# Kernel optimization log

Hardware: AMD Instinct MI355X
Metric: run time of the kernel (lower is better)

## Reference

```python
import jax, jax.numpy as jnp
import numpy as np

N_FFT = 4096
HOP = 1024
EPS = 1e-10


def hann(n):
    # periodic Hann window, matches torch.hann_window(n)
    return 0.5 - 0.5 * jnp.cos(2.0 * jnp.pi * jnp.arange(n) / n)


def stft(x, window):
    # x: (..., T) real -> (..., F, frames) complex; center=True, reflect pad, onesided
    pad = N_FFT // 2
    x = jnp.pad(x, [(0, 0)] * (x.ndim - 1) + [(pad, pad)], mode='reflect')
    n_frames = 1 + (x.shape[-1] - N_FFT) // HOP
    idx = jnp.arange(n_frames)[:, None] * HOP + jnp.arange(N_FFT)[None, :]
    frames = x[..., idx] * window  # (..., frames, N_FFT)
    return jnp.swapaxes(jnp.fft.rfft(frames, axis=-1), -1, -2)  # (..., F, frames)


def istft(spec, window, length):
    # spec: (..., F, frames) complex -> (..., length) real; torch.istft semantics (center=True)
    frames = jnp.fft.irfft(jnp.swapaxes(spec, -1, -2), n=N_FFT, axis=-1) * window
    n_frames = frames.shape[-2]
    out_len = N_FFT + HOP * (n_frames - 1)
    idx = (jnp.arange(n_frames)[:, None] * HOP + jnp.arange(N_FFT)[None, :]).reshape(-1)
    flat = frames.reshape(frames.shape[:-2] + (-1,))
    y = jnp.zeros(frames.shape[:-2] + (out_len,), frames.dtype).at[..., idx].add(flat)
    wsq = jnp.zeros((out_len,), frames.dtype).at[idx].add(jnp.tile(window ** 2, n_frames))
    y = y / jnp.where(wsq > 1e-11, wsq, 1.0)
    pad = N_FFT // 2
    return y[..., pad:pad + length]


def setup_inputs() -> dict:
    key = jax.random.key(0)
    k1, k2, k3 = jax.random.split(key, 3)
    audio = jax.random.normal(k1, (2, 2, 441000), jnp.float32)
    W = jax.random.normal(k2, (4, 2049, 2049), jnp.float32) * 0.02
    b = jax.random.normal(k3, (4, 2049), jnp.float32) * 0.01
    return {"audio": audio, "W": W, "b": b}


def reference(audio, W, b):
    window = hann(N_FFT).astype(audio.dtype)
    mix = stft(audio, window)                 # (N, C, F, T) complex64
    X = jnp.abs(mix)                          # ComplexNorm, mono=False, power=1
    Xd = jax.lax.stop_gradient(X)             # Separator feeds X.detach() to target models
    # target models: per-target linear over frequency bins + ReLU (nonneg spectrogram)
    V = jax.nn.relu(jnp.einsum('ncft,jgf->njcgt', Xd, W) + b[None, :, None, :, None])
    # wiener(iterations=0, softmask=False, residual=False): y_j = v_j * exp(i*angle(mix))
    phase = mix / (jnp.abs(mix) + EPS)        # unit-magnitude complex
    Y = V.astype(phase.real.dtype) * phase[:, None]  # (N, J, C, F, T) complex
    estimates = istft(Y, window, audio.shape[-1])    # (N, J, C, T_audio)
    return estimates
```

## Files before the change

kernel.cpp:

```cpp
#include <hip/hip_runtime.h>
#include <hip/hip_bf16.h>
#include <math.h>

#define T_AUDIO 441000
#define NH   2048
#define HOP  1024
#define NBINS 2049
#define NFRAMES 431
#define PAD  2048

#define GP  2176
#define KP  2112
#define TPN 512

#define NBLK 108
#define SPAN 7168

#define TWO_PI 6.2831853071795864769f

#define PADI(i) ((i) + ((i) >> 4))

typedef __bf16 bf16_t;
typedef bf16_t bf16x8 __attribute__((ext_vector_type(8)));
typedef bf16_t bf16x4 __attribute__((ext_vector_type(4)));
typedef float f32x4 __attribute__((ext_vector_type(4)));
typedef _Float16 h16;
typedef h16 h16x4 __attribute__((ext_vector_type(4)));

__device__ __forceinline__ unsigned pack_bf2(float a, float b) {
    union { bf16_t h; unsigned short u; } ca, cb;
    ca.h = (bf16_t)a; cb.h = (bf16_t)b;
    return (unsigned)ca.u | ((unsigned)cb.u << 16);
}
__device__ __forceinline__ float2 unpack_bf2(unsigned v) {
    union { unsigned u; float f; } a, b;
    a.u = v << 16;
    b.u = v & 0xffff0000u;
    return make_float2(a.f, b.f);
}

__device__ __forceinline__ float2 cadd(float2 a, float2 b) { return make_float2(a.x + b.x, a.y + b.y); }
__device__ __forceinline__ float2 csub(float2 a, float2 b) { return make_float2(a.x - b.x, a.y - b.y); }
__device__ __forceinline__ float2 cmul(float2 a, float2 b) {
    return make_float2(a.x * b.x - a.y * b.y, a.x * b.y + a.y * b.x);
}
__device__ __forceinline__ float2 cmulc(float2 u, float2 w) {
    return make_float2(u.x * w.x + u.y * w.y, u.y * w.x - u.x * w.y);
}

__global__ void k_tab(float2* __restrict__ tw) {
    int i = blockIdx.x * 256 + threadIdx.x;
    if (i < 4096) {
        float s, c;
        sincosf((float)i * (TWO_PI / 4096.0f), &s, &c);
        tw[i] = make_float2(c, s);
    }
}

template<bool FWD>
__device__ __forceinline__ void fft2048_reg8(float2* x, int tid,
                                             const float2* __restrict__ tw) {
    const float sgn = FWD ? -1.0f : 1.0f;
    const float R2 = 0.70710678118654752440f;
    int s = 1, ls = 0, fac = 2;
    #pragma unroll
    for (int st = 0; st < 3; st++) {
        int q = tid & (s - 1);
        int p = tid >> ls;
        int e = p * fac;
        float2 w[7];
        #pragma unroll
        for (int k = 0; k < 7; k++) w[k] = tw[e * (k + 1)];
        float2 v[8];
        #pragma unroll
        for (int k = 0; k < 8; k++) v[k] = x[PADI(tid + 256 * k)];
        __syncthreads();
        float2 s0 = cadd(v[0], v[4]), s1 = cadd(v[1], v[5]),
               s2 = cadd(v[2], v[6]), s3 = cadd(v[3], v[7]);
        float2 d0 = csub(v[0], v[4]), d1 = csub(v[1], v[5]),
               d2 = csub(v[2], v[6]), d3 = csub(v[3], v[7]);
        float2 X0, X1, X2, X3, X4, X5, X6, X7;
        {
            float2 t0 = cadd(s0, s2), t1 = csub(s0, s2);
            float2 t2 = cadd(s1, s3), t3 = csub(s1, s3);
            float2 it3 = make_float2(-sgn * t3.y, sgn * t3.x);
            X0 = cadd(t0, t2); X4 = csub(t0, t2);
            X2 = cadd(t1, it3); X6 = csub(t1, it3);
        }
        {
            float2 e0 = d0;
            float2 e1 = make_float2(R2 * (d1.x - sgn * d1.y), R2 * (sgn * d1.x + d1.y));
            float2 e2 = make_float2(-sgn * d2.y, sgn * d2.x);
            float2 e3 = make_float2(-R2 * (d3.x + sgn * d3.y), R2 * (sgn * d3.x - d3.y));
            float2 t0 = cadd(e0, e2), t1 = csub(e0, e2);
            float2 t2 = cadd(e1, e3), t3 = csub(e1, e3);
            float2 it3 = make_float2(-sgn * t3.y, sgn * t3.x);
            X1 = cadd(t0, t2); X5 = csub(t0, t2);
            X3 = cadd(t1, it3); X7 = csub(t1, it3);
        }
        int ob = q + 8 * s * p;
        x[PADI(ob)] = X0;
        float2 XX[7] = {X1, X2, X3, X4, X5, X6, X7};
        #pragma unroll
        for (int k = 0; k < 7; k++) {
            float2 u = XX[k];
            x[PADI(ob + s * (k + 1))] = FWD ? cmulc(u, w[k]) : cmul(w[k], u);
        }
        __syncthreads();
        s <<= 3; ls += 3; fac <<= 3;
    }
    {
        float2 v[8];
        #pragma unroll
        for (int k = 0; k < 8; k++) v[k] = x[PADI(tid + 256 * k)];
        __syncthreads();
        #pragma unroll
        for (int h = 0; h < 2; h++) {
            float2 c0 = v[h], c1 = v[h + 2], c2 = v[h + 4], c3 = v[h + 6];
            float2 t0 = cadd(c0, c2), t1 = csub(c0, c2);
            float2 t2 = cadd(c1, c3), t3 = csub(c1, c3);
            float2 it3 = make_float2(-sgn * t3.y, sgn * t3.x);
            int base = tid + 256 * h;
            x[PADI(base)]        = cadd(t0, t2);
            x[PADI(base + 512)]  = cadd(t1, it3);
            x[PADI(base + 1024)] = csub(t0, t2);
            x[PADI(base + 1536)] = csub(t1, it3);
        }
        __syncthreads();
    }
}

__global__ __launch_bounds__(256) void k_stft(const float* __restrict__ audio,
        bf16_t* __restrict__ Xb, unsigned* __restrict__ ph,
        const float2* __restrict__ tw) {
    __shared__ float2 buf[2176];
    int blk = blockIdx.x;
    int nc = blk / NFRAMES;
    int fr = blk - nc * NFRAMES;
    const float* a = audio + (size_t)nc * T_AUDIO;
    int tid = threadIdx.x;
    int base = fr * HOP - PAD;
    #pragma unroll
    for (int it = 0; it < 8; it++) {
        int m = tid + it * 256;
        int r0 = base + 2 * m;
        int r1 = r0 + 1;
        r0 = r0 < 0 ? -r0 : (r0 >= T_AUDIO ? 2 * T_AUDIO - 2 - r0 : r0);
        r1 = r1 < 0 ? -r1 : (r1 >= T_AUDIO ? 2 * T_AUDIO - 2 - r1 : r1);
        float4 tt = ((const float4*)tw)[m];
        float x0 = a[r0] * (0.5f - 0.5f * tt.x);
        float x1 = a[r1] * (0.5f - 0.5f * tt.z);
        buf[PADI(m)] = make_float2(x0, x1);
    }
    __syncthreads();
    fft2048_reg8<true>(buf, tid, tw);
    size_t orow = ((size_t)nc * NFRAMES + fr) * KP;
    bf16_t* Xrow = Xb + ((size_t)nc * TPN + fr) * KP;
    for (int k = tid; k < NBINS; k += 256) {
        float2 Zk = buf[PADI(k & 2047)];
        float2 Zm = buf[PADI((2048 - k) & 2047)];
        float ex = 0.5f * (Zk.x + Zm.x), ey = 0.5f * (Zk.y - Zm.y);
        float ox = 0.5f * (Zk.y + Zm.y), oy = -0.5f * (Zk.x - Zm.x);
        float2 w = tw[k];
        float re = ex + w.x * ox + w.y * oy;
        float im = ey + w.x * oy - w.y * ox;
        float mag = sqrtf(re * re + im * im);
        float inv = 1.0f / (mag + 1e-10f);
        Xrow[k] = (bf16_t)mag;
        ph[orow + k] = pack_bf2(re * inv, im * inv);
    }
}

__global__ __launch_bounds__(256) void k_convW(const float* __restrict__ W,
        bf16_t* __restrict__ Wb) {
    size_t idx = (size_t)blockIdx.x * 256 + threadIdx.x;
    size_t total = (size_t)4 * GP * KP / 8;
    if (idx >= total) return;
    size_t e = idx * 8;
    int f0 = (int)(e % KP);
    size_t rem = e / KP;
    int g = (int)(rem % GP);
    int j = (int)(rem / GP);
    bf16x8 v = {};
    if (g < NBINS) {
        const float* src = W + ((size_t)j * NBINS + g) * NBINS;
        #pragma unroll
        for (int r = 0; r < 8; r++) {
            int f = f0 + r;
            v[r] = (bf16_t)(f < NBINS ? src[f] : 0.0f);
        }
    }
    *(bf16x8*)(Wb + e) = v;
}

__global__ __launch_bounds__(256) void k_gemm_mfma(const bf16_t* __restrict__ Wb,
        const float* __restrict__ bias, const bf16_t* __restrict__ Xb,
        bf16_t* __restrict__ V) {
    __shared__ bf16_t As[128 * 64];
    __shared__ bf16_t Bs[64 * 64];
    int id = blockIdx.x;
    int xcd = id & 7, nn = id >> 3;
    int G = xcd + 8 * (nn / 28);
    if (G >= 68) return;
    int m28 = nn % 28;
    int j  = G / 17;
    int g0 = (G % 17) * 128;
    int nc = m28 / 7;
    int t0 = (m28 % 7) * 64;
    const bf16_t* A = Wb + ((size_t)j * GP + g0) * KP;
    const bf16_t* B = Xb + ((size_t)nc * TPN + t0) * KP;
    int tid = threadIdx.x;
    int lane = tid & 63, wid = tid >> 6;
    int wm = wid >> 1, wn = wid & 1;

    const bf16_t* srcA[4];
    #pragma unroll
    for (int i = 0; i < 4; i++) {
        int s = i * 256 + tid;
        int r = s >> 3, cc = (s & 7) ^ (r & 7);
        srcA[i] = A + (size_t)r * KP + cc * 8;
    }
    const bf16_t* srcB[2];
    #pragma unroll
    for (int i = 0; i < 2; i++) {
        int s = i * 256 + tid;
        int r = s >> 3, cc = (s & 7) ^ (r & 7);
        srcB[i] = B + (size_t)r * KP + cc * 8;
    }

    int laneLo = lane & 15, laneHi = lane >> 4;
    int offA[4][2], offB[2][2];
    #pragma unroll
    for (int mm = 0; mm < 4; mm++) {
        int r = wm * 64 + mm * 16 + laneLo;
        #pragma unroll
        for (int kk = 0; kk < 2; kk++) {
            int c = kk * 4 + laneHi;
            offA[mm][kk] = r * 128 + ((c ^ (r & 7)) << 4);
        }
    }
    #pragma unroll
    for (int n = 0; n < 2; n++) {
        int r = wn * 32 + n * 16 + laneLo;
        #pragma unroll
        for (int kk = 0; kk < 2; kk++) {
            int c = kk * 4 + laneHi;
            offB[n][kk] = r * 128 + ((c ^ (r & 7)) << 4);
        }
    }

    f32x4 acc[4][2];
    #pragma unroll
    for (int mm = 0; mm < 4; mm++)
        #pragma unroll
        for (int n = 0; n < 2; n++)
            acc[mm][n] = (f32x4){0.f, 0.f, 0.f, 0.f};

    for (int k0 = 0; k0 < KP; k0 += 64) {
        #pragma unroll
        for (int i = 0; i < 4; i++)
            __builtin_amdgcn_global_load_lds(
                (const __attribute__((address_space(1))) void*)(srcA[i] + k0),
                (__attribute__((address_space(3))) void*)(As + (i * 256 + tid) * 8),
                16, 0, 0);
        #pragma unroll
        for (int i = 0; i < 2; i++)
            __builtin_amdgcn_global_load_lds(
                (const __attribute__((address_space(1))) void*)(srcB[i] + k0),
                (__attribute__((address_space(3))) void*)(Bs + (i * 256 + tid) * 8),
                16, 0, 0);
        __syncthreads();

        bf16x8 af[4][2], bfr[2][2];
        #pragma unroll
        for (int mm = 0; mm < 4; mm++)
            #pragma unroll
            for (int kk = 0; kk < 2; kk++)
                af[mm][kk] = *(const bf16x8*)((const char*)As + offA[mm][kk]);
        #pragma unroll
        for (int n = 0; n < 2; n++)
            #pragma unroll
            for (int kk = 0; kk < 2; kk++)
                bfr[n][kk] = *(const bf16x8*)((const char*)Bs + offB[n][kk]);
        #pragma unroll
        for (int mm = 0; mm < 4; mm++)
            #pragma unroll
            for (int n = 0; n < 2; n++)
                #pragma unroll
                for (int kk = 0; kk < 2; kk++)
                    acc[mm][n] = __builtin_amdgcn_mfma_f32_16x16x32_bf16(
                        af[mm][kk], bfr[n][kk], acc[mm][n], 0, 0, 0);
        __syncthreads();
    }

    int jnc = j * 4 + nc;
    int colT = laneLo;
    int rowB = laneHi * 4;
    #pragma unroll
    for (int n = 0; n < 2; n++) {
        int t = t0 + wn * 32 + n * 16 + colT;
        if (t >= NFRAMES) continue;
        size_t vrow = ((size_t)jnc * NFRAMES + t) * KP;
        #pragma unroll
        for (int mm = 0; mm < 4; mm++) {
            int g = g0 + wm * 64 + mm * 16 + rowB;
            if (g + 3 < NBINS) {
                bf16x4 o;
                #pragma unroll
                for (int r = 0; r < 4; r++)
                    o[r] = (bf16_t)fmaxf(acc[mm][n][r] + bias[j * NBINS + g + r], 0.0f);
                *(bf16x4*)(V + vrow + g) = o;
            } else {
                #pragma unroll
                for (int r = 0; r < 4; r++) {
                    int gg = g + r;
                    if (gg < NBINS)
                        V[vrow + gg] = (bf16_t)fmaxf(acc[mm][n][r] + bias[j * NBINS + gg], 0.0f);
                }
            }
        }
    }
}

__global__ __launch_bounds__(256) void k_istft(const bf16_t* __restrict__ V,
        const unsigned* __restrict__ ph, const float2* __restrict__ tw,
        h16* __restrict__ strips) {
    __shared__ float2 buf[2176];
    __shared__ float accS[SPAN];
    int b = blockIdx.x, njc = blockIdx.y;
    int n = njc >> 3, j = (njc >> 1) & 3, c = njc & 1;
    int nc = n * 2 + c;
    int jnc = j * 4 + nc;
    int tid = threadIdx.x;
    #pragma unroll
    for (int i = tid; i < SPAN / 4; i += 256)
        ((float4*)accS)[i] = make_float4(0.f, 0.f, 0.f, 0.f);

    for (int p = 0; p < 4; p++) {
        int fr = b * 4 + p;
        if (fr >= NFRAMES) break;
        size_t vrow = ((size_t)jnc * NFRAMES + fr) * KP;
        size_t prow = ((size_t)nc * NFRAMES + fr) * KP;
        #pragma unroll
        for (int it = 0; it < 8; it++) {
            int k = tid + it * 256;
            int km = 2048 - k;
            float vk = (float)V[vrow + k];
            float2 pk = unpack_bf2(ph[prow + k]);
            float vm = (float)V[vrow + km];
            float2 pm = unpack_bf2(ph[prow + km]);
            float2 Yk = make_float2(vk * pk.x, vk * pk.y);
            float2 Ym = make_float2(vm * pm.x, vm * pm.y);
            float ex = 0.5f * (Yk.x + Ym.x), ey = 0.5f * (Yk.y - Ym.y);
            float wx = 0.5f * (Yk.x - Ym.x), wy = 0.5f * (Yk.y + Ym.y);
            float2 w = tw[k];
            float ox_ = w.x * wx - w.y * wy;
            float oy_ = w.x * wy + w.y * wx;
            buf[PADI(k)] = make_float2(ex - oy_, ey + ox_);
        }
        __syncthreads();
        fft2048_reg8<false>(buf, tid, tw);
        const float scale = 1.0f / 2048.0f;
        #pragma unroll
        for (int it = 0; it < 8; it++) {
            int m = tid + it * 256;
            float2 z = buf[PADI(m)];
            float4 tt = ((const float4*)tw)[m];
            int o = p * 1024 + 2 * m;
            accS[o]     += z.x * scale * (0.5f - 0.5f * tt.x);
            accS[o + 1] += z.y * scale * (0.5f - 0.5f * tt.z);
        }
        __syncthreads();
    }
    h16* dst = strips + ((size_t)njc * NBLK + b) * SPAN;
    for (int i = tid; i < SPAN / 4; i += 256) {
        float4 v = ((float4*)accS)[i];
        h16x4 o = { (h16)v.x, (h16)v.y, (h16)v.z, (h16)v.w };
        *(h16x4*)(dst + i * 4) = o;
    }
}

__global__ __launch_bounds__(256) void k_final(const h16* __restrict__ strips,
        const float2* __restrict__ tw, float* __restrict__ out) {
    int gidx = blockIdx.x * 256 + threadIdx.x;
    int t = gidx * 2;
    if (t >= T_AUDIO) return;
    int njc = blockIdx.y;
    const h16* S = strips + (size_t)njc * NBLK * SPAN;
    float o[2];
    #pragma unroll
    for (int u = 0; u < 2; u++) {
        int tt = t + u;
        int q = tt + PAD;
        int b1 = q >> 12, o1 = q & 4095;
        float s = 0.f;
        if (b1 < NBLK) s += (float)S[b1 * SPAN + o1];
        if (b1 > 0 && o1 < SPAN - 4096) s += (float)S[(b1 - 1) * SPAN + o1 + 4096];
        float wsq;
        if (tt >= 1024 && tt <= 439295) {
            wsq = 1.5f;
        } else {
            wsq = 0.f;
            int ib = q >> 10;
            #pragma unroll
            for (int d = 0; d < 4; d++) {
                int i = ib - d;
                if (i >= 0 && i < NFRAMES) {
                    int m = q - (i << 10);
                    float w = 0.5f - 0.5f * tw[m].x;
                    wsq += w * w;
                }
            }
            if (!(wsq > 1e-11f)) wsq = 1.f;
        }
        o[u] = s / wsq;
    }
    *(float2*)(out + (size_t)njc * T_AUDIO + t) = make_float2(o[0], o[1]);
}

extern "C" void kernel_launch(void* const* d_in, const int* in_sizes, int n_in,
                              void* d_out, int out_size, void* d_ws, size_t ws_size,
                              hipStream_t stream) {
    const float* audio = (const float*)d_in[0];
    const float* Wm    = (const float*)d_in[1];
    const float* bias  = (const float*)d_in[2];
    float* out = (float*)d_out;
    char* ws = (char*)d_ws;

    size_t szWb  = (size_t)4 * GP * KP * sizeof(bf16_t);
    size_t szXb  = (size_t)4 * TPN * KP * sizeof(bf16_t);
    size_t szPh  = (size_t)4 * NFRAMES * KP * sizeof(unsigned);
    size_t szV   = (size_t)16 * NFRAMES * KP * sizeof(bf16_t);
    size_t szStr = (size_t)16 * NBLK * SPAN * sizeof(h16);
    size_t szTw  = (size_t)4096 * sizeof(float2);

    bf16_t*   Wb    = (bf16_t*)ws;   ws += szWb;
    bf16_t*   Xb    = (bf16_t*)ws;   ws += szXb;
    unsigned* ph    = (unsigned*)ws; ws += szPh;
    bf16_t*   V     = (bf16_t*)ws;   ws += szV;
    h16*      strips= (h16*)ws;      ws += szStr;
    float2*   tw    = (float2*)ws;   ws += szTw;
    if ((size_t)(ws - (char*)d_ws) > ws_size) return;

    hipMemsetAsync(Xb, 0, szXb, stream);

    k_tab<<<dim3(16), 256, 0, stream>>>(tw);
    k_convW<<<dim3((unsigned)((4ull * GP * KP / 8 + 255) / 256)), 256, 0, stream>>>(Wm, Wb);
    k_stft<<<dim3(4 * NFRAMES), 256, 0, stream>>>(audio, Xb, ph, tw);
    k_gemm_mfma<<<dim3(2016), 256, 0, stream>>>(Wb, bias, Xb, V);
    k_istft<<<dim3(NBLK, 16), 256, 0, stream>>>(V, ph, tw, strips);
    k_final<<<dim3((T_AUDIO / 2 + 255) / 256, 16), 256, 0, stream>>>(strips, tw, out);
}
```

Baseline: 255.4 us.

## Enlarge GEMM tile to 128x128 over packed frames and fold twiddle table into convW

```diff
diff --git a/kernel.cpp b/kernel.cpp
--- a/kernel.cpp
+++ b/kernel.cpp
@@ -11,7 +11,7 @@
 
 #define GP  2176
 #define KP  2112
-#define TPN 512
+#define TPN 448
 
 #define NBLK 108
 #define SPAN 7168
@@ -46,15 +46,6 @@
 }
 __device__ __forceinline__ float2 cmulc(float2 u, float2 w) {
     return make_float2(u.x * w.x + u.y * w.y, u.y * w.x - u.x * w.y);
-}
-
-__global__ void k_tab(float2* __restrict__ tw) {
-    int i = blockIdx.x * 256 + threadIdx.x;
-    if (i < 4096) {
-        float s, c;
-        sincosf((float)i * (TWO_PI / 4096.0f), &s, &c);
-        tw[i] = make_float2(c, s);
-    }
 }
 
 template<bool FWD>
@@ -172,7 +163,13 @@
 }
 
 __global__ __launch_bounds__(256) void k_convW(const float* __restrict__ W,
-        bf16_t* __restrict__ Wb) {
+        bf16_t* __restrict__ Wb, float2* __restrict__ tw) {
+    if (blockIdx.x < 16) {
+        int i = blockIdx.x * 256 + threadIdx.x;
+        float s, c;
+        sincosf((float)i * (TWO_PI / 4096.0f), &s, &c);
+        tw[i] = make_float2(c, s);
+    }
     size_t idx = (size_t)blockIdx.x * 256 + threadIdx.x;
     size_t total = (size_t)4 * GP * KP / 8;
     if (idx >= total) return;
@@ -197,39 +194,33 @@
         const float* __restrict__ bias, const bf16_t* __restrict__ Xb,
         bf16_t* __restrict__ V) {
     __shared__ bf16_t As[128 * 64];
-    __shared__ bf16_t Bs[64 * 64];
+    __shared__ bf16_t Bs[128 * 64];
     int id = blockIdx.x;
     int xcd = id & 7, nn = id >> 3;
-    int G = xcd + 8 * (nn / 28);
+    int G = xcd + 8 * (nn / 14);
     if (G >= 68) return;
-    int m28 = nn % 28;
+    int mblk = nn % 14;
     int j  = G / 17;
     int g0 = (G % 17) * 128;
-    int nc = m28 / 7;
-    int t0 = (m28 % 7) * 64;
+    int t0 = mblk * 128;
     const bf16_t* A = Wb + ((size_t)j * GP + g0) * KP;
-    const bf16_t* B = Xb + ((size_t)nc * TPN + t0) * KP;
+    const bf16_t* B = Xb + (size_t)t0 * KP;
     int tid = threadIdx.x;
     int lane = tid & 63, wid = tid >> 6;
     int wm = wid >> 1, wn = wid & 1;
 
     const bf16_t* srcA[4];
+    const bf16_t* srcB[4];
     #pragma unroll
     for (int i = 0; i < 4; i++) {
         int s = i * 256 + tid;
         int r = s >> 3, cc = (s & 7) ^ (r & 7);
         srcA[i] = A + (size_t)r * KP + cc * 8;
-    }
-    const bf16_t* srcB[2];
-    #pragma unroll
-    for (int i = 0; i < 2; i++) {
-        int s = i * 256 + tid;
-        int r = s >> 3, cc = (s & 7) ^ (r & 7);
         srcB[i] = B + (size_t)r * KP + cc * 8;
     }
 
     int laneLo = lane & 15, laneHi = lane >> 4;
-    int offA[4][2], offB[2][2];
+    int offA[4][2], offB[4][2];
     #pragma unroll
     for (int mm = 0; mm < 4; mm++) {
         int r = wm * 64 + mm * 16 + laneLo;
@@ -240,8 +231,8 @@
         }
     }
     #pragma unroll
-    for (int n = 0; n < 2; n++) {
-        int r = wn * 32 + n * 16 + laneLo;
+    for (int n = 0; n < 4; n++) {
+        int r = wn * 64 + n * 16 + laneLo;
         #pragma unroll
         for (int kk = 0; kk < 2; kk++) {
             int c = kk * 4 + laneHi;
@@ -249,11 +240,11 @@
         }
     }
 
-    f32x4 acc[4][2];
+    f32x4 acc[4][4];
     #pragma unroll
     for (int mm = 0; mm < 4; mm++)
         #pragma unroll
-        for (int n = 0; n < 2; n++)
+        for (int n = 0; n < 4; n++)
             acc[mm][n] = (f32x4){0.f, 0.f, 0.f, 0.f};
 
     for (int k0 = 0; k0 < KP; k0 += 64) {
@@ -264,43 +255,41 @@
                 (__attribute__((address_space(3))) void*)(As + (i * 256 + tid) * 8),
                 16, 0, 0);
         #pragma unroll
-        for (int i = 0; i < 2; i++)
+        for (int i = 0; i < 4; i++)
             __builtin_amdgcn_global_load_lds(
                 (const __attribute__((address_space(1))) void*)(srcB[i] + k0),
                 (__attribute__((address_space(3))) void*)(Bs + (i * 256 + tid) * 8),
                 16, 0, 0);
         __syncthreads();
 
-        bf16x8 af[4][2], bfr[2][2];
-        #pragma unroll
-        for (int mm = 0; mm < 4; mm++)
+        #pragma unroll
+        for (int kk = 0; kk < 2; kk++) {
+            bf16x8 af[4], bfr[4];
             #pragma unroll
-            for (int kk = 0; kk < 2; kk++)
-                af[mm][kk] = *(const bf16x8*)((const char*)As + offA[mm][kk]);
-        #pragma unroll
-        for (int n = 0; n < 2; n++)
+            for (int mm = 0; mm < 4; mm++)
+                af[mm] = *(const bf16x8*)((const char*)As + offA[mm][kk]);
             #pragma unroll
-            for (int kk = 0; kk < 2; kk++)
-                bfr[n][kk] = *(const bf16x8*)((const char*)Bs + offB[n][kk]);
-        #pragma unroll
-        for (int mm = 0; mm < 4; mm++)
+            for (int n = 0; n < 4; n++)
+                bfr[n] = *(const bf16x8*)((const char*)Bs + offB[n][kk]);
             #pragma unroll
-            for (int n = 0; n < 2; n++)
+            for (int mm = 0; mm < 4; mm++)
                 #pragma unroll
-                for (int kk = 0; kk < 2; kk++)
+                for (int n = 0; n < 4; n++)
                     acc[mm][n] = __builtin_amdgcn_mfma_f32_16x16x32_bf16(
-                        af[mm][kk], bfr[n][kk], acc[mm][n], 0, 0, 0);
-        __syncthreads();
-    }
-
-    int jnc = j * 4 + nc;
+                        af[mm], bfr[n], acc[mm][n], 0, 0, 0);
+        }
+        __syncthreads();
+    }
+
     int colT = laneLo;
     int rowB = laneHi * 4;
     #pragma unroll
-    for (int n = 0; n < 2; n++) {
-        int t = t0 + wn * 32 + n * 16 + colT;
-        if (t >= NFRAMES) continue;
-        size_t vrow = ((size_t)jnc * NFRAMES + t) * KP;
+    for (int n = 0; n < 4; n++) {
+        int t = t0 + wn * 64 + n * 16 + colT;
+        int nc = t / TPN;
+        int tl = t - nc * TPN;
+        if (tl >= NFRAMES) continue;
+        size_t vrow = (((size_t)(j * 4 + nc)) * NFRAMES + tl) * KP;
         #pragma unroll
         for (int mm = 0; mm < 4; mm++) {
             int g = g0 + wm * 64 + mm * 16 + rowB;
@@ -444,10 +433,9 @@
 
     hipMemsetAsync(Xb, 0, szXb, stream);
 
-    k_tab<<<dim3(16), 256, 0, stream>>>(tw);
-    k_convW<<<dim3((unsigned)((4ull * GP * KP / 8 + 255) / 256)), 256, 0, stream>>>(Wm, Wb);
+    k_convW<<<dim3((unsigned)((4ull * GP * KP / 8 + 255) / 256)), 256, 0, stream>>>(Wm, Wb, tw);
     k_stft<<<dim3(4 * NFRAMES), 256, 0, stream>>>(audio, Xb, ph, tw);
-    k_gemm_mfma<<<dim3(2016), 256, 0, stream>>>(Wb, bias, Xb, V);
+    k_gemm_mfma<<<dim3(72 * 14), 256, 0, stream>>>(Wb, bias, Xb, V);
     k_istft<<<dim3(NBLK, 16), 256, 0, stream>>>(V, ph, tw, strips);
     k_final<<<dim3((T_AUDIO / 2 + 255) / 256, 16), 256, 0, stream>>>(strips, tw, out);
 }
```

Result: no change. 255.1 us (-0.1%).

## Accumulate iSTFT overlap in registers, fold twiddle table into convW, drop barriers

Applied to the files above, without the earlier changes.

```diff
diff --git a/kernel.cpp b/kernel.cpp
--- a/kernel.cpp
+++ b/kernel.cpp
@@ -11,7 +11,7 @@
 
 #define GP  2176
 #define KP  2112
-#define TPN 512
+#define TPN 448
 
 #define NBLK 108
 #define SPAN 7168
@@ -25,7 +25,7 @@
 typedef bf16_t bf16x4 __attribute__((ext_vector_type(4)));
 typedef float f32x4 __attribute__((ext_vector_type(4)));
 typedef _Float16 h16;
-typedef h16 h16x4 __attribute__((ext_vector_type(4)));
+typedef h16 h16x2 __attribute__((ext_vector_type(2)));
 
 __device__ __forceinline__ unsigned pack_bf2(float a, float b) {
     union { bf16_t h; unsigned short u; } ca, cb;
@@ -46,15 +46,6 @@
 }
 __device__ __forceinline__ float2 cmulc(float2 u, float2 w) {
     return make_float2(u.x * w.x + u.y * w.y, u.y * w.x - u.x * w.y);
-}
-
-__global__ void k_tab(float2* __restrict__ tw) {
-    int i = blockIdx.x * 256 + threadIdx.x;
-    if (i < 4096) {
-        float s, c;
-        sincosf((float)i * (TWO_PI / 4096.0f), &s, &c);
-        tw[i] = make_float2(c, s);
-    }
 }
 
 template<bool FWD>
@@ -152,7 +143,6 @@
         float x1 = a[r1] * (0.5f - 0.5f * tt.z);
         buf[PADI(m)] = make_float2(x0, x1);
     }
-    __syncthreads();
     fft2048_reg8<true>(buf, tid, tw);
     size_t orow = ((size_t)nc * NFRAMES + fr) * KP;
     bf16_t* Xrow = Xb + ((size_t)nc * TPN + fr) * KP;
@@ -172,7 +162,13 @@
 }
 
 __global__ __launch_bounds__(256) void k_convW(const float* __restrict__ W,
-        bf16_t* __restrict__ Wb) {
+        bf16_t* __restrict__ Wb, float2* __restrict__ tw) {
+    if (blockIdx.x < 16) {
+        int i = blockIdx.x * 256 + threadIdx.x;
+        float s, c;
+        sincosf((float)i * (TWO_PI / 4096.0f), &s, &c);
+        tw[i] = make_float2(c, s);
+    }
     size_t idx = (size_t)blockIdx.x * 256 + threadIdx.x;
     size_t total = (size_t)4 * GP * KP / 8;
     if (idx >= total) return;
@@ -326,57 +322,55 @@
         const unsigned* __restrict__ ph, const float2* __restrict__ tw,
         h16* __restrict__ strips) {
     __shared__ float2 buf[2176];
-    __shared__ float accS[SPAN];
     int b = blockIdx.x, njc = blockIdx.y;
     int n = njc >> 3, j = (njc >> 1) & 3, c = njc & 1;
     int nc = n * 2 + c;
     int jnc = j * 4 + nc;
     int tid = threadIdx.x;
-    #pragma unroll
-    for (int i = tid; i < SPAN / 4; i += 256)
-        ((float4*)accS)[i] = make_float4(0.f, 0.f, 0.f, 0.f);
-
+    const float scale = 1.0f / 2048.0f;
+    float2 acc[14];
+    #pragma unroll
+    for (int u = 0; u < 14; u++) acc[u] = make_float2(0.f, 0.f);
+
+    #pragma unroll
     for (int p = 0; p < 4; p++) {
         int fr = b * 4 + p;
-        if (fr >= NFRAMES) break;
-        size_t vrow = ((size_t)jnc * NFRAMES + fr) * KP;
-        size_t prow = ((size_t)nc * NFRAMES + fr) * KP;
-        #pragma unroll
-        for (int it = 0; it < 8; it++) {
-            int k = tid + it * 256;
-            int km = 2048 - k;
-            float vk = (float)V[vrow + k];
-            float2 pk = unpack_bf2(ph[prow + k]);
-            float vm = (float)V[vrow + km];
-            float2 pm = unpack_bf2(ph[prow + km]);
-            float2 Yk = make_float2(vk * pk.x, vk * pk.y);
-            float2 Ym = make_float2(vm * pm.x, vm * pm.y);
-            float ex = 0.5f * (Yk.x + Ym.x), ey = 0.5f * (Yk.y - Ym.y);
-            float wx = 0.5f * (Yk.x - Ym.x), wy = 0.5f * (Yk.y + Ym.y);
-            float2 w = tw[k];
-            float ox_ = w.x * wx - w.y * wy;
-            float oy_ = w.x * wy + w.y * wx;
-            buf[PADI(k)] = make_float2(ex - oy_, ey + ox_);
-        }
-        __syncthreads();
-        fft2048_reg8<false>(buf, tid, tw);
-        const float scale = 1.0f / 2048.0f;
-        #pragma unroll
-        for (int it = 0; it < 8; it++) {
-            int m = tid + it * 256;
-            float2 z = buf[PADI(m)];
-            float4 tt = ((const float4*)tw)[m];
-            int o = p * 1024 + 2 * m;
-            accS[o]     += z.x * scale * (0.5f - 0.5f * tt.x);
-            accS[o + 1] += z.y * scale * (0.5f - 0.5f * tt.z);
-        }
-        __syncthreads();
+        if (fr < NFRAMES) {
+            size_t vrow = ((size_t)jnc * NFRAMES + fr) * KP;
+            size_t prow = ((size_t)nc * NFRAMES + fr) * KP;
+            #pragma unroll
+            for (int it = 0; it < 8; it++) {
+                int k = tid + it * 256;
+                int km = 2048 - k;
+                float vk = (float)V[vrow + k];
+                float2 pk = unpack_bf2(ph[prow + k]);
+                float vm = (float)V[vrow + km];
+                float2 pm = unpack_bf2(ph[prow + km]);
+                float2 Yk = make_float2(vk * pk.x, vk * pk.y);
+                float2 Ym = make_float2(vm * pm.x, vm * pm.y);
+                float ex = 0.5f * (Yk.x + Ym.x), ey = 0.5f * (Yk.y - Ym.y);
+                float wx = 0.5f * (Yk.x - Ym.x), wy = 0.5f * (Yk.y + Ym.y);
+                float2 w = tw[k];
+                float ox_ = w.x * wx - w.y * wy;
+                float oy_ = w.x * wy + w.y * wx;
+                buf[PADI(k)] = make_float2(ex - oy_, ey + ox_);
+            }
+            fft2048_reg8<false>(buf, tid, tw);
+            #pragma unroll
+            for (int it = 0; it < 8; it++) {
+                int m = tid + it * 256;
+                float2 z = buf[PADI(m)];
+                float4 tt = ((const float4*)tw)[m];
+                acc[2 * p + it].x += z.x * scale * (0.5f - 0.5f * tt.x);
+                acc[2 * p + it].y += z.y * scale * (0.5f - 0.5f * tt.z);
+            }
+        }
     }
     h16* dst = strips + ((size_t)njc * NBLK + b) * SPAN;
-    for (int i = tid; i < SPAN / 4; i += 256) {
-        float4 v = ((float4*)accS)[i];
-        h16x4 o = { (h16)v.x, (h16)v.y, (h16)v.z, (h16)v.w };
-        *(h16x4*)(dst + i * 4) = o;
+    #pragma unroll
+    for (int u = 0; u < 14; u++) {
+        h16x2 o = { (h16)acc[u].x, (h16)acc[u].y };
+        *(h16x2*)(dst + 512 * u + 2 * tid) = o;
     }
 }
 
@@ -444,10 +438,9 @@
 
     hipMemsetAsync(Xb, 0, szXb, stream);
 
-    k_tab<<<dim3(16), 256, 0, stream>>>(tw);
-    k_convW<<<dim3((unsigned)((4ull * GP * KP / 8 + 255) / 256)), 256, 0, stream>>>(Wm, Wb);
+    k_convW<<<dim3((unsigned)((4ull * GP * KP / 8 + 255) / 256)), 256, 0, stream>>>(Wm, Wb, tw);
     k_stft<<<dim3(4 * NFRAMES), 256, 0, stream>>>(audio, Xb, ph, tw);
-    k_gemm_mfma<<<dim3(2016), 256, 0, stream>>>(Wb, bias, Xb, V);
+    k_gemm_mfma<<<dim3(72 * 28), 256, 0, stream>>>(Wb, bias, Xb, V);
     k_istft<<<dim3(NBLK, 16), 256, 0, stream>>>(V, ph, tw, strips);
     k_final<<<dim3((T_AUDIO / 2 + 255) / 256, 16), 256, 0, stream>>>(strips, tw, out);
 }
```

After: 243.9 us. -4.5%, faster.
